# Kernel optimization log

Measured on AMD Instinct MI355X. Metric: run time of the kernel, lower is better.

## Reference

```python
import jax, jax.numpy as jnp
import numpy as np

N_NODES = 50000
N_EDGES = 800000
D_NODE = 64
D_EDGE = 64
D_OUT = 64
D_HID = 128
LN_EPS = 1e-5


def _mlp_params(key, d_in):
    # layer sizes: [d_in, D_HID, D_HID, D_OUT]; weights stored [in, out]
    ks = jax.random.split(key, 3)
    dims = [d_in, D_HID, D_HID, D_OUT]
    params = []
    for i in range(3):
        s = 1.0 / np.sqrt(dims[i])
        params.append(jax.random.uniform(ks[i], (dims[i], dims[i + 1]), minval=-s, maxval=s, dtype=jnp.float32))
        params.append(jnp.zeros((dims[i + 1],), jnp.float32))
    # LayerNorm gamma/beta
    params.append(jnp.ones((D_OUT,), jnp.float32))
    params.append(jnp.zeros((D_OUT,), jnp.float32))
    return params


def _mlp_ln(h, W0, b0, W1, b1, W2, b2, g, beta):
    h = jax.nn.relu(h @ W0 + b0)
    h = jax.nn.relu(h @ W1 + b1)
    h = h @ W2 + b2
    mu = jnp.mean(h, axis=-1, keepdims=True)
    var = jnp.mean(jnp.square(h - mu), axis=-1, keepdims=True)
    return (h - mu) * jax.lax.rsqrt(var + LN_EPS) * g + beta


def setup_inputs() -> dict:
    key = jax.random.key(0)
    k = jax.random.split(key, 8)
    inp = {
        "x": jax.random.normal(k[0], (N_NODES, D_NODE), jnp.float32),
        "mesh_edge_index": jax.random.randint(k[1], (2, N_EDGES), 0, N_NODES, dtype=jnp.int32),
        "mesh_edge_attr": jax.random.normal(k[2], (N_EDGES, D_EDGE), jnp.float32),
        "world_edge_index": jax.random.randint(k[3], (2, N_EDGES), 0, N_NODES, dtype=jnp.int32),
        "world_edge_attr": jax.random.normal(k[4], (N_EDGES, D_EDGE), jnp.float32),
    }
    names = ["W0", "b0", "W1", "b1", "W2", "b2", "ln_g", "ln_b"]
    for pref, kk, d_in in [("mesh", k[5], 2 * D_NODE + D_EDGE),
                           ("world", k[6], 2 * D_NODE + D_EDGE),
                           ("upd", k[7], D_NODE + 2 * D_OUT)]:
        ps = _mlp_params(kk, d_in)
        for nm, p in zip(names, ps):
            inp[f"{pref}_{nm}"] = p
    return inp


def _edge_block(x, edge_index, edge_attr, W0, b0, W1, b1, W2, b2, g, beta):
    src, dst = edge_index[0], edge_index[1]  # PyG: x_j = source, x_i = target
    x_i = x[dst]  # [E, D_NODE]
    x_j = x[src]
    concat = jnp.concatenate([x_i, x_j, edge_attr], axis=-1)  # [E, 2D+De]
    new_edge = edge_attr + _mlp_ln(concat, W0, b0, W1, b1, W2, b2, g, beta)
    agg = jax.ops.segment_sum(new_edge, dst, num_segments=N_NODES)  # 'add' aggr at target
    return agg, new_edge


def reference(x, mesh_edge_index, mesh_edge_attr, world_edge_index, world_edge_attr,
              mesh_W0, mesh_b0, mesh_W1, mesh_b1, mesh_W2, mesh_b2, mesh_ln_g, mesh_ln_b,
              world_W0, world_b0, world_W1, world_b1, world_W2, world_b2, world_ln_g, world_ln_b,
              upd_W0, upd_b0, upd_W1, upd_b1, upd_W2, upd_b2, upd_ln_g, upd_ln_b):
    agg_m, new_edge_m = _edge_block(x, mesh_edge_index, mesh_edge_attr,
                                    mesh_W0, mesh_b0, mesh_W1, mesh_b1, mesh_W2, mesh_b2, mesh_ln_g, mesh_ln_b)
    agg_w, new_edge_w = _edge_block(x, world_edge_index, world_edge_attr,
                                    world_W0, world_b0, world_W1, world_b1, world_W2, world_b2, world_ln_g, world_ln_b)
    concat = jnp.concatenate([x, agg_m, agg_w], axis=-1)  # [N, D_NODE + 2*D_OUT]
    x_new = x + _mlp_ln(concat, upd_W0, upd_b0, upd_W1, upd_b1, upd_W2, upd_b2, upd_ln_g, upd_ln_b)
    return x_new, new_edge_m, new_edge_w
```

## Files before the change

kernel.cpp:

```cpp
#include <hip/hip_runtime.h>


#define NNODES 50000
#define NEDGES 800000
#define NBLK 512

typedef __bf16 bf16x8 __attribute__((ext_vector_type(8)));
typedef float f32x4 __attribute__((ext_vector_type(4)));
#define MFMA(a, b, c) __builtin_amdgcn_mfma_f32_16x16x32_bf16(a, b, c, 0, 0, 0)

#define OFF_A 0
#define OFF_H0 24576
#define OFF_P 40960
#define OFF_PAR 43008
#define SMEM 44800

__device__ __forceinline__ unsigned short f2bf(float f) {
  unsigned u = __builtin_bit_cast(unsigned, f);
  u = (u + 0x7fffu + ((u >> 16) & 1u)) >> 16;
  return (unsigned short)u;
}
__device__ __forceinline__ unsigned long long pk4(f32x4 v) {
  union { unsigned short h[4]; unsigned long long u; } p;
  p.h[0] = f2bf(v[0]); p.h[1] = f2bf(v[1]); p.h[2] = f2bf(v[2]); p.h[3] = f2bf(v[3]);
  return p.u;
}
__device__ __forceinline__ int4 pk8(float4 a, float4 b) {
  union { unsigned short us[8]; int4 v; } u;
  u.us[0] = f2bf(a.x); u.us[1] = f2bf(a.y); u.us[2] = f2bf(a.z); u.us[3] = f2bf(a.w);
  u.us[4] = f2bf(b.x); u.us[5] = f2bf(b.y); u.us[6] = f2bf(b.z); u.us[7] = f2bf(b.w);
  return u.v;
}
__device__ __forceinline__ int4 ldpk(const float* p) {
  return pk8(*(const float4*)p, *(const float4*)(p + 4));
}

template <bool EDGE>
__global__ __launch_bounds__(512, 4) void mlp_block(
    const float* __restrict__ g1, const float* __restrict__ g2,
    const float* __restrict__ g3, const int* __restrict__ srcI,
    const int* __restrict__ dstI, const unsigned short* __restrict__ Wt,
    const float* __restrict__ b0, const float* __restrict__ b1,
    const float* __restrict__ b2, const float* __restrict__ gam,
    const float* __restrict__ bet, float* __restrict__ outp, int M) {
  __shared__ __align__(16) char sm[SMEM];
  const int tid = threadIdx.x, lane = tid & 63, wave = tid >> 6;
  const int lrow = lane & 15, cg = lane >> 4;
  const unsigned short* Wt0 = Wt;
  const unsigned short* Wt1 = Wt + 24576;
  const unsigned short* Wt2 = Wt + 40960;
  const int ntiles = (M + 63) >> 6;
  const int cg2 = wave & 3, rg = wave >> 2;

  for (int i = tid; i < 448; i += 512) {
    float v;
    if (i < 128) v = b0[i];
    else if (i < 256) v = b1[i - 128];
    else if (i < 320) v = b2[i - 256];
    else if (i < 384) v = gam[i - 320];
    else v = bet[i - 384];
    ((float*)(sm + OFF_PAR))[i] = v;
  }
  const float* PAR = (const float*)(sm + OFF_PAR);

  bf16x8 w0f[6], w1f[4], w2f[4];
#pragma unroll
  for (int kk = 0; kk < 6; ++kk)
    w0f[kk] = *(const bf16x8*)(Wt0 + (wave * 16 + lrow) * 192 + kk * 32 + cg * 8);
#pragma unroll
  for (int kk = 0; kk < 4; ++kk)
    w1f[kk] = *(const bf16x8*)(Wt1 + (wave * 16 + lrow) * 128 + kk * 32 + cg * 8);
#pragma unroll
  for (int kk = 0; kk < 4; ++kk)
    w2f[kk] = *(const bf16x8*)(Wt2 + (cg2 * 16 + lrow) * 128 + kk * 32 + cg * 8);

  const int srow = (tid >> 5) * 4 + ((tid & 31) >> 3), oct = tid & 7;

  int4 pxd, pxs, pat;
  auto LOADT = [&](int tt) {
    const int row = tt * 64 + srow;
    if (EDGE) {
      const int d = dstI[row], s = srcI[row];
      pxd = ldpk(g1 + (size_t)d * 64 + oct * 8);
      pxs = ldpk(g1 + (size_t)s * 64 + oct * 8);
      pat = ldpk(g3 + (size_t)row * 64 + oct * 8);
    } else {
      const int rr = min(row, M - 1);
      pxd = ldpk(g1 + (size_t)rr * 64 + oct * 8);
      pxs = ldpk(g2 + (size_t)rr * 64 + oct * 8);
      pat = ldpk(g3 + (size_t)rr * 64 + oct * 8);
    }
  };
  auto STAGE = [&]() {
    char* a0 = sm + OFF_A + srow * 384;
    const int swz = (srow & 7) << 4;
    *(int4*)(a0 + ((oct * 16) ^ swz)) = pxd;
    *(int4*)(a0 + ((128 + oct * 16) ^ swz)) = pxs;
    *(int4*)(a0 + ((256 + oct * 16) ^ swz)) = pat;
  };

  int t = blockIdx.x;
  if (t >= ntiles) return;
  LOADT(t);
  STAGE();

  for (; t < ntiles; t += NBLK) {
    const int tn = t + NBLK;
    const bool more = tn < ntiles;
    __syncthreads();
    if (more) LOADT(tn);
    {
      const f32x4 bb0 = *(const f32x4*)(PAR + wave * 16 + cg * 4);
#pragma unroll
      for (int rt = 0; rt < 4; ++rt) {
        const int row = rt * 16 + lrow, swz = (row & 7) << 4;
        const char* ab = sm + OFF_A + row * 384;
        f32x4 acc = {0.f, 0.f, 0.f, 0.f};
#pragma unroll
        for (int kk = 0; kk < 6; ++kk)
          acc = MFMA(w0f[kk], *(const bf16x8*)(ab + ((kk * 64 + cg * 16) ^ swz)), acc);
        f32x4 h;
#pragma unroll
        for (int q = 0; q < 4; ++q) h[q] = fmaxf(acc[q] + bb0[q], 0.f);
        *(unsigned long long*)(sm + OFF_H0 + row * 256 + ((wave * 32 + cg * 8) ^ swz)) = pk4(h);
      }
    }
    __syncthreads();
    {
      const f32x4 bb1 = *(const f32x4*)(PAR + 128 + wave * 16 + cg * 4);
#pragma unroll
      for (int rt = 0; rt < 4; ++rt) {
        const int row = rt * 16 + lrow, swz = (row & 7) << 4;
        const char* hb = sm + OFF_H0 + row * 256;
        f32x4 acc = {0.f, 0.f, 0.f, 0.f};
#pragma unroll
        for (int kk = 0; kk < 4; ++kk)
          acc = MFMA(w1f[kk], *(const bf16x8*)(hb + ((kk * 64 + cg * 16) ^ swz)), acc);
        f32x4 h;
#pragma unroll
        for (int q = 0; q < 4; ++q) h[q] = fmaxf(acc[q] + bb1[q], 0.f);
        *(unsigned long long*)(sm + OFF_A + row * 384 + ((wave * 32 + cg * 8) ^ swz)) = pk4(h);
      }
    }
    __syncthreads();
    f32x4 accE[2];
    {
      const f32x4 bb2 = *(const f32x4*)(PAR + 256 + cg2 * 16 + cg * 4);
#pragma unroll
      for (int j = 0; j < 2; ++j) {
        const int row = (rg * 2 + j) * 16 + lrow, swz = (row & 7) << 4;
        const char* hb = sm + OFF_A + row * 384;
        f32x4 acc = {0.f, 0.f, 0.f, 0.f};
#pragma unroll
        for (int kk = 0; kk < 4; ++kk)
          acc = MFMA(w2f[kk], *(const bf16x8*)(hb + ((kk * 64 + cg * 16) ^ swz)), acc);
#pragma unroll
        for (int q = 0; q < 4; ++q) acc[q] += bb2[q];
        float s = acc[0] + acc[1] + acc[2] + acc[3];
        float ss = acc[0] * acc[0] + acc[1] * acc[1] + acc[2] * acc[2] + acc[3] * acc[3];
        s += __shfl_xor(s, 16, 64); s += __shfl_xor(s, 32, 64);
        ss += __shfl_xor(ss, 16, 64); ss += __shfl_xor(ss, 32, 64);
        if (cg == 0) *(float2*)(sm + OFF_P + row * 32 + cg2 * 8) = make_float2(s, ss);
        accE[j] = acc;
      }
    }
    __syncthreads();
    {
      const f32x4 gv = *(const f32x4*)(PAR + 320 + cg2 * 16 + cg * 4);
      const f32x4 bv = *(const f32x4*)(PAR + 384 + cg2 * 16 + cg * 4);
#pragma unroll
      for (int j = 0; j < 2; ++j) {
        const int row = (rg * 2 + j) * 16 + lrow, gr = t * 64 + row;
        float4 p0 = *(const float4*)(sm + OFF_P + row * 32);
        float4 p1 = *(const float4*)(sm + OFF_P + row * 32 + 16);
        float s = p0.x + p0.z + p1.x + p1.z, ss = p0.y + p0.w + p1.y + p1.w;
        float mean = s * (1.f / 64.f);
        float var = fmaxf(ss * (1.f / 64.f) - mean * mean, 0.f);
        float inv = rsqrtf(var + 1e-5f);
        const int col = cg2 * 16 + cg * 4;
        const int grc = EDGE ? gr : min(gr, M - 1);
        const f32x4 r = *(const f32x4*)(g3 + (size_t)grc * 64 + col);
        f32x4 a = accE[j], o;
#pragma unroll
        for (int q = 0; q < 4; ++q) o[q] = (a[q] - mean) * inv * gv[q] + bv[q] + r[q];
        if (EDGE || gr < M) *(f32x4*)(outp + (size_t)gr * 64 + col) = o;
      }
    }
    if (more) STAGE();
  }
}

__global__ __launch_bounds__(256) void agg_k(const float* __restrict__ oute,
                                             const int* __restrict__ perm,
                                             const int* __restrict__ rp,
                                             float* __restrict__ agg) {
  const int lane = threadIdx.x & 63;
  const int r4 = lane >> 4, cq = lane & 15;
  const int w = (blockIdx.x * 256 + threadIdx.x) >> 6;
  const int nw = gridDim.x * 4;
  for (int d = w; d < NNODES; d += nw) {
    const int s = rp[d], e = rp[d + 1];
    f32x4 acc = {0.f, 0.f, 0.f, 0.f};
    for (int j = s + r4; j < e; j += 4) {
      const int row = perm[j];
      const f32x4 v = *(const f32x4*)(oute + (size_t)row * 64 + cq * 4);
#pragma unroll
      for (int q = 0; q < 4; ++q) acc[q] += v[q];
    }
#pragma unroll
    for (int q = 0; q < 4; ++q) {
      acc[q] += __shfl_xor(acc[q], 16, 64);
      acc[q] += __shfl_xor(acc[q], 32, 64);
    }
    if (r4 == 0) *(f32x4*)(agg + (size_t)d * 64 + cq * 4) = acc;
  }
}

struct PrepArgs { const float* w[9]; unsigned short* wt[3]; };

__global__ void prep_w(PrepArgs pa) {
  int i = blockIdx.x * 256 + threadIdx.x;
  if (i >= 3 * 49152) return;
  int mlp = i / 49152;
  int rem = i - mlp * 49152;
  int mat, off, K, N;
  if (rem < 24576)      { mat = 0; off = 0;     K = 192; N = 128; }
  else if (rem < 40960) { mat = 1; off = 24576; K = 128; N = 128; }
  else                  { mat = 2; off = 40960; K = 128; N = 64;  }
  int local = rem - off;
  int n = local / K, k = local - n * K;
  if (mlp == 2 && mat == 0) k = (k + 64) % 192;
  pa.wt[mlp][rem] = f2bf(pa.w[mlp * 3 + mat][k * N + n]);
}

__global__ void zero_f4(float4* p, int n) {
  int i = blockIdx.x * blockDim.x + threadIdx.x;
  if (i < n) p[i] = make_float4(0.f, 0.f, 0.f, 0.f);
}

__global__ void hist_k(const int* __restrict__ dM, const int* __restrict__ dW,
                       int* __restrict__ curM, int* __restrict__ curW, int E) {
  int i = blockIdx.x * 256 + threadIdx.x;
  if (i < E) {
    atomicAdd(curM + dM[i], 1);
    atomicAdd(curW + dW[i], 1);
  }
}

__global__ __launch_bounds__(1024) void scan_k(int* __restrict__ curM, int* __restrict__ curW,
                                               int* __restrict__ rpM, int* __restrict__ rpW) {
  __shared__ int buf[1024];
  int* cur = blockIdx.x ? curW : curM;
  int* rp = blockIdx.x ? rpW : rpM;
  const int tid = threadIdx.x, base = tid * 49;
  const int lim = min(base + 49, NNODES);
  int p = 0;
  for (int b = base; b < lim; ++b) p += cur[b];
  buf[tid] = p;
  __syncthreads();
  const int own = p;
  for (int off = 1; off < 1024; off <<= 1) {
    int nv = (tid >= off) ? buf[tid - off] : 0;
    __syncthreads();
    buf[tid] += nv;
    __syncthreads();
  }
  int running = buf[tid] - own;
  for (int b = base; b < lim; ++b) {
    int h = cur[b];
    cur[b] = running;
    rp[b] = running;
    running += h;
  }
  if (tid == 1023) rp[NNODES] = buf[1023];
}

__global__ void scatter_k(const int* __restrict__ dM, const int* __restrict__ dW,
                          int* __restrict__ curM, int* __restrict__ curW,
                          int* __restrict__ permM, int* __restrict__ permW, int E) {
  int i = blockIdx.x * 256 + threadIdx.x;
  if (i < E) {
    int p = atomicAdd(curM + dM[i], 1);
    permM[p] = i;
    p = atomicAdd(curW + dW[i], 1);
    permW[p] = i;
  }
}

extern "C" void kernel_launch(void* const* d_in, const int* in_sizes, int n_in,
                              void* d_out, int out_size, void* d_ws, size_t ws_size,
                              hipStream_t stream) {
  const float* x      = (const float*)d_in[0];
  const int*   meIdx  = (const int*)d_in[1];
  const float* meAttr = (const float*)d_in[2];
  const int*   weIdx  = (const int*)d_in[3];
  const float* weAttr = (const float*)d_in[4];

  float* out_x  = (float*)d_out;
  float* out_em = out_x + (size_t)NNODES * 64;
  float* out_ew = out_em + (size_t)NEDGES * 64;

  char* ws = (char*)d_ws;
  unsigned short* WtM = (unsigned short*)ws;
  unsigned short* WtW = (unsigned short*)(ws + 98304);
  unsigned short* WtU = (unsigned short*)(ws + 196608);
  float* aggm = (float*)(ws + 294912);
  float* aggw = aggm + (size_t)NNODES * 64;
  char* p = ws + 294912 + 25600000;
  int* curM  = (int*)p;
  int* curW  = curM + NNODES;
  int* rpM   = (int*)(p + 400000);
  int* rpW   = rpM + 50016;
  int* permM = rpW + 50016;
  int* permW = permM + NEDGES;

  zero_f4<<<dim3(98), dim3(256), 0, stream>>>((float4*)curM, 25000);

  PrepArgs pa;
  for (int m = 0; m < 3; ++m)
    for (int l = 0; l < 3; ++l)
      pa.w[m * 3 + l] = (const float*)d_in[5 + m * 8 + l * 2];
  pa.wt[0] = WtM; pa.wt[1] = WtW; pa.wt[2] = WtU;
  prep_w<<<dim3(576), dim3(256), 0, stream>>>(pa);

  hist_k<<<dim3(3125), dim3(256), 0, stream>>>(meIdx + NEDGES, weIdx + NEDGES, curM, curW, NEDGES);
  scan_k<<<dim3(2), dim3(1024), 0, stream>>>(curM, curW, rpM, rpW);
  scatter_k<<<dim3(3125), dim3(256), 0, stream>>>(meIdx + NEDGES, weIdx + NEDGES,
                                                  curM, curW, permM, permW, NEDGES);

  mlp_block<true><<<dim3(NBLK), dim3(512), 0, stream>>>(
      x, x, meAttr, meIdx, meIdx + NEDGES, WtM,
      (const float*)d_in[6], (const float*)d_in[8], (const float*)d_in[10],
      (const float*)d_in[11], (const float*)d_in[12],
      out_em, NEDGES);
  mlp_block<true><<<dim3(NBLK), dim3(512), 0, stream>>>(
      x, x, weAttr, weIdx, weIdx + NEDGES, WtW,
      (const float*)d_in[14], (const float*)d_in[16], (const float*)d_in[18],
      (const float*)d_in[19], (const float*)d_in[20],
      out_ew, NEDGES);

  agg_k<<<dim3(1024), dim3(256), 0, stream>>>(out_em, permM, rpM, aggm);
  agg_k<<<dim3(1024), dim3(256), 0, stream>>>(out_ew, permW, rpW, aggw);

  mlp_block<false><<<dim3(NBLK), dim3(512), 0, stream>>>(
      aggm, aggw, x, nullptr, nullptr, WtU,
      (const float*)d_in[22], (const float*)d_in[24], (const float*)d_in[26],
      (const float*)d_in[27], (const float*)d_in[28],
      out_x, NNODES);
}
```

Baseline: 931.5 us.

## Pre-convert x to bf16, merge mesh/world edge MLP and aggregation launches

Adds a prep kernel that converts node features to bf16 once, so the edge MLP gathers half-width rows and skips per-edge conversion. The mesh and world edge MLPs now run as one launch of twice as many blocks selected by block index, and the two aggregation launches merge into one. The aggregation loop also prefetches the next permutation index. This trades an extra small kernel and more workspace for fewer launches, better occupancy overlap and less gather traffic.

After: 922.9 us. No clear change (-0.9%).

```diff
diff --git a/kernel.cpp b/kernel.cpp
--- a/kernel.cpp
+++ b/kernel.cpp
@@ -35,15 +35,33 @@
   return pk8(*(const float4*)p, *(const float4*)(p + 4));
 }
 
+struct MArgs {
+  const float* g1[2];
+  const float* g2[2];
+  const float* attrf[2];
+  const unsigned short* xb;
+  const int* src[2];
+  const int* dst[2];
+  const unsigned short* Wt[2];
+  const float* b0[2]; const float* b1[2]; const float* b2[2];
+  const float* gm[2]; const float* bt[2];
+  float* outp[2];
+};
+
 template <bool EDGE>
-__global__ __launch_bounds__(512, 4) void mlp_block(
-    const float* __restrict__ g1, const float* __restrict__ g2,
-    const float* __restrict__ g3, const int* __restrict__ srcI,
-    const int* __restrict__ dstI, const unsigned short* __restrict__ Wt,
-    const float* __restrict__ b0, const float* __restrict__ b1,
-    const float* __restrict__ b2, const float* __restrict__ gam,
-    const float* __restrict__ bet, float* __restrict__ outp, int M) {
+__global__ __launch_bounds__(512, 4) void mlp_block(MArgs a, int M) {
   __shared__ __align__(16) char sm[SMEM];
+  const int set = EDGE ? (int)(blockIdx.x >= NBLK) : 0;
+  const int bid0 = blockIdx.x - set * NBLK;
+  const float* g1 = a.g1[set];
+  const float* g2 = a.g2[set];
+  const float* attrf = a.attrf[set];
+  const unsigned short* xb = a.xb;
+  const int* srcI = a.src[set];
+  const int* dstI = a.dst[set];
+  const unsigned short* Wt = a.Wt[set];
+  float* outp = a.outp[set];
+
   const int tid = threadIdx.x, lane = tid & 63, wave = tid >> 6;
   const int lrow = lane & 15, cg = lane >> 4;
   const unsigned short* Wt0 = Wt;
@@ -54,11 +72,11 @@
 
   for (int i = tid; i < 448; i += 512) {
     float v;
-    if (i < 128) v = b0[i];
-    else if (i < 256) v = b1[i - 128];
-    else if (i < 320) v = b2[i - 256];
-    else if (i < 384) v = gam[i - 320];
-    else v = bet[i - 384];
+    if (i < 128) v = a.b0[set][i];
+    else if (i < 256) v = a.b1[set][i - 128];
+    else if (i < 320) v = a.b2[set][i - 256];
+    else if (i < 384) v = a.gm[set][i - 320];
+    else v = a.bt[set][i - 384];
     ((float*)(sm + OFF_PAR))[i] = v;
   }
   const float* PAR = (const float*)(sm + OFF_PAR);
@@ -80,15 +98,15 @@
   auto LOADT = [&](int tt) {
     const int row = tt * 64 + srow;
     if (EDGE) {
-      const int d = dstI[row], s = srcI[row];
-      pxd = ldpk(g1 + (size_t)d * 64 + oct * 8);
-      pxs = ldpk(g1 + (size_t)s * 64 + oct * 8);
-      pat = ldpk(g3 + (size_t)row * 64 + oct * 8);
+      const int d = dstI[row], s2 = srcI[row];
+      pxd = *(const int4*)(xb + (size_t)d * 64 + oct * 8);
+      pxs = *(const int4*)(xb + (size_t)s2 * 64 + oct * 8);
+      pat = ldpk(attrf + (size_t)row * 64 + oct * 8);
     } else {
       const int rr = min(row, M - 1);
       pxd = ldpk(g1 + (size_t)rr * 64 + oct * 8);
       pxs = ldpk(g2 + (size_t)rr * 64 + oct * 8);
-      pat = ldpk(g3 + (size_t)rr * 64 + oct * 8);
+      pat = *(const int4*)(xb + (size_t)rr * 64 + oct * 8);
     }
   };
   auto STAGE = [&]() {
@@ -99,7 +117,7 @@
     *(int4*)(a0 + ((256 + oct * 16) ^ swz)) = pat;
   };
 
-  int t = blockIdx.x;
+  int t = bid0;
   if (t >= ntiles) return;
   LOADT(t);
   STAGE();
@@ -179,10 +197,10 @@
         float inv = rsqrtf(var + 1e-5f);
         const int col = cg2 * 16 + cg * 4;
         const int grc = EDGE ? gr : min(gr, M - 1);
-        const f32x4 r = *(const f32x4*)(g3 + (size_t)grc * 64 + col);
-        f32x4 a = accE[j], o;
-#pragma unroll
-        for (int q = 0; q < 4; ++q) o[q] = (a[q] - mean) * inv * gv[q] + bv[q] + r[q];
+        const f32x4 r = *(const f32x4*)(attrf + (size_t)grc * 64 + col);
+        f32x4 av = accE[j], o;
+#pragma unroll
+        for (int q = 0; q < 4; ++q) o[q] = (av[q] - mean) * inv * gv[q] + bv[q] + r[q];
         if (EDGE || gr < M) *(f32x4*)(outp + (size_t)gr * 64 + col) = o;
       }
     }
@@ -190,28 +208,42 @@
   }
 }
 
-__global__ __launch_bounds__(256) void agg_k(const float* __restrict__ oute,
-                                             const int* __restrict__ perm,
-                                             const int* __restrict__ rp,
-                                             float* __restrict__ agg) {
+__global__ __launch_bounds__(256) void agg_k(const float* __restrict__ em,
+                                             const float* __restrict__ ew,
+                                             const int* __restrict__ permM,
+                                             const int* __restrict__ permW,
+                                             const int* __restrict__ rpM,
+                                             const int* __restrict__ rpW,
+                                             float* __restrict__ aggm,
+                                             float* __restrict__ aggw) {
   const int lane = threadIdx.x & 63;
   const int r4 = lane >> 4, cq = lane & 15;
   const int w = (blockIdx.x * 256 + threadIdx.x) >> 6;
   const int nw = gridDim.x * 4;
-  for (int d = w; d < NNODES; d += nw) {
+  for (int dd = w; dd < 2 * NNODES; dd += nw) {
+    const bool s1 = dd >= NNODES;
+    const int d = s1 ? dd - NNODES : dd;
+    const float* oute = s1 ? ew : em;
+    const int* perm = s1 ? permW : permM;
+    const int* rp = s1 ? rpW : rpM;
     const int s = rp[d], e = rp[d + 1];
     f32x4 acc = {0.f, 0.f, 0.f, 0.f};
-    for (int j = s + r4; j < e; j += 4) {
-      const int row = perm[j];
-      const f32x4 v = *(const f32x4*)(oute + (size_t)row * 64 + cq * 4);
+    int j = s + r4;
+    int row0 = (j < e) ? perm[j] : -1;
+    while (row0 >= 0) {
+      const int j1 = j + 4;
+      const int row1 = (j1 < e) ? perm[j1] : -1;
+      const f32x4 v = *(const f32x4*)(oute + (size_t)row0 * 64 + cq * 4);
 #pragma unroll
       for (int q = 0; q < 4; ++q) acc[q] += v[q];
+      row0 = row1; j = j1;
     }
 #pragma unroll
     for (int q = 0; q < 4; ++q) {
       acc[q] += __shfl_xor(acc[q], 16, 64);
       acc[q] += __shfl_xor(acc[q], 32, 64);
     }
+    float* agg = s1 ? aggw : aggm;
     if (r4 == 0) *(f32x4*)(agg + (size_t)d * 64 + cq * 4) = acc;
   }
 }
@@ -231,6 +263,11 @@
   int n = local / K, k = local - n * K;
   if (mlp == 2 && mat == 0) k = (k + 64) % 192;
   pa.wt[mlp][rem] = f2bf(pa.w[mlp * 3 + mat][k * N + n]);
+}
+
+__global__ void prep_x(const float* __restrict__ x, unsigned short* __restrict__ xb) {
+  int i = blockIdx.x * 256 + threadIdx.x;
+  if (i < NNODES * 8) *(int4*)(xb + (size_t)i * 8) = ldpk(x + (size_t)i * 8);
 }
 
 __global__ void zero_f4(float4* p, int n) {
@@ -304,9 +341,10 @@
   unsigned short* WtM = (unsigned short*)ws;
   unsigned short* WtW = (unsigned short*)(ws + 98304);
   unsigned short* WtU = (unsigned short*)(ws + 196608);
-  float* aggm = (float*)(ws + 294912);
-  float* aggw = aggm + (size_t)NNODES * 64;
-  char* p = ws + 294912 + 25600000;
+  unsigned short* xb  = (unsigned short*)(ws + 294912);
+  float* aggm = (float*)(ws + 6694912);
+  float* aggw = (float*)(ws + 19494912);
+  char* p = ws + 32294912;
   int* curM  = (int*)p;
   int* curW  = curM + NNODES;
   int* rpM   = (int*)(p + 400000);
@@ -322,29 +360,39 @@
       pa.w[m * 3 + l] = (const float*)d_in[5 + m * 8 + l * 2];
   pa.wt[0] = WtM; pa.wt[1] = WtW; pa.wt[2] = WtU;
   prep_w<<<dim3(576), dim3(256), 0, stream>>>(pa);
+  prep_x<<<dim3(1563), dim3(256), 0, stream>>>(x, xb);
 
   hist_k<<<dim3(3125), dim3(256), 0, stream>>>(meIdx + NEDGES, weIdx + NEDGES, curM, curW, NEDGES);
   scan_k<<<dim3(2), dim3(1024), 0, stream>>>(curM, curW, rpM, rpW);
   scatter_k<<<dim3(3125), dim3(256), 0, stream>>>(meIdx + NEDGES, weIdx + NEDGES,
                                                   curM, curW, permM, permW, NEDGES);
 
-  mlp_block<true><<<dim3(NBLK), dim3(512), 0, stream>>>(
-      x, x, meAttr, meIdx, meIdx + NEDGES, WtM,
-      (const float*)d_in[6], (const float*)d_in[8], (const float*)d_in[10],
-      (const float*)d_in[11], (const float*)d_in[12],
-      out_em, NEDGES);
-  mlp_block<true><<<dim3(NBLK), dim3(512), 0, stream>>>(
-      x, x, weAttr, weIdx, weIdx + NEDGES, WtW,
-      (const float*)d_in[14], (const float*)d_in[16], (const float*)d_in[18],
-      (const float*)d_in[19], (const float*)d_in[20],
-      out_ew, NEDGES);
-
-  agg_k<<<dim3(1024), dim3(256), 0, stream>>>(out_em, permM, rpM, aggm);
-  agg_k<<<dim3(1024), dim3(256), 0, stream>>>(out_ew, permW, rpW, aggw);
-
-  mlp_block<false><<<dim3(NBLK), dim3(512), 0, stream>>>(
-      aggm, aggw, x, nullptr, nullptr, WtU,
-      (const float*)d_in[22], (const float*)d_in[24], (const float*)d_in[26],
-      (const float*)d_in[27], (const float*)d_in[28],
-      out_x, NNODES);
-}
+  MArgs ea = {};
+  ea.xb = xb;
+  ea.attrf[0] = meAttr;          ea.attrf[1] = weAttr;
+  ea.src[0] = meIdx;             ea.src[1] = weIdx;
+  ea.dst[0] = meIdx + NEDGES;    ea.dst[1] = weIdx + NEDGES;
+  ea.Wt[0] = WtM;                ea.Wt[1] = WtW;
+  ea.b0[0] = (const float*)d_in[6];   ea.b0[1] = (const float*)d_in[14];
+  ea.b1[0] = (const float*)d_in[8];   ea.b1[1] = (const float*)d_in[16];
+  ea.b2[0] = (const float*)d_in[10];  ea.b2[1] = (const float*)d_in[18];
+  ea.gm[0] = (const float*)d_in[11];  ea.gm[1] = (const float*)d_in[19];
+  ea.bt[0] = (const float*)d_in[12];  ea.bt[1] = (const float*)d_in[20];
+  ea.outp[0] = out_em;           ea.outp[1] = out_ew;
+  mlp_block<true><<<dim3(2 * NBLK), dim3(512), 0, stream>>>(ea, NEDGES);
+
+  agg_k<<<dim3(2048), dim3(256), 0, stream>>>(out_em, out_ew, permM, permW, rpM, rpW, aggm, aggw);
+
+  MArgs na = {};
+  na.xb = xb;
+  na.g1[0] = aggm; na.g2[0] = aggw;
+  na.attrf[0] = x;
+  na.Wt[0] = WtU;
+  na.b0[0] = (const float*)d_in[22];
+  na.b1[0] = (const float*)d_in[24];
+  na.b2[0] = (const float*)d_in[26];
+  na.gm[0] = (const float*)d_in[27];
+  na.bt[0] = (const float*)d_in[28];
+  na.outp[0] = out_x;
+  mlp_block<false><<<dim3(NBLK), dim3(512), 0, stream>>>(na, NNODES);
+}
```
